# Optimization experiments

Measured on AMD Instinct MI355X. Metric: run time of the kernel, lower is better.

Reference implementation:

```python
import jax, jax.numpy as jnp
import numpy as np

B, T, C, H = 4, 4096, 1024, 64

def setup_inputs() -> dict:
    key = jax.random.key(0)
    kx, kq, kk, kv = jax.random.split(key, 4)
    x = jax.random.normal(kx, (B, T, C), dtype=jnp.float32)
    scale = 1.0 / np.sqrt(C)
    Wq = jax.random.normal(kq, (C, H), dtype=jnp.float32) * scale
    Wk = jax.random.normal(kk, (C, H), dtype=jnp.float32) * scale
    Wv = jax.random.normal(kv, (C, H), dtype=jnp.float32) * scale
    return {"x": x, "Wq": Wq, "Wk": Wk, "Wv": Wv}

def reference(x, Wq, Wk, Wv):
    Bsz, Tlen, _ = x.shape
    head_size = Wq.shape[1]
    q = x @ Wq  # [B,T,H]
    k = x @ Wk
    v = x @ Wv
    # scores [B,T,T], scaled by sqrt(head_size)
    scores = jnp.einsum('bqh,bkh->bqk', q, k) / jnp.sqrt(jnp.float32(head_size))
    causal = jnp.tril(jnp.ones((Tlen, Tlen), dtype=bool))
    scores = jnp.where(causal, scores, -jnp.inf)
    weights = jax.nn.softmax(scores, axis=-1)
    # dropout p=0.0 -> identity
    return jnp.einsum('bqk,bkh->bqh', weights, v)
```

## Files before the change

### kernel.cpp

```cpp
#include <hip/hip_runtime.h>
#include <hip/hip_bf16.h>

typedef __attribute__((ext_vector_type(8))) short short8;
typedef __attribute__((ext_vector_type(4))) float f32x4;

#define MFMA16(a, b, c) __builtin_amdgcn_mfma_f32_16x16x32_bf16((a), (b), (c), 0, 0, 0)

typedef const __attribute__((address_space(1))) unsigned int* gas_t;
typedef __attribute__((address_space(3))) unsigned int* las_t;
#define GLDS16(g, l) __builtin_amdgcn_global_load_lds((gas_t)(g), (las_t)(l), 16, 0, 0)

__device__ inline unsigned short f2bf(float f) {
    union { float f; unsigned int u; } v;
    v.f = f;
    unsigned int u = v.u;
    return (unsigned short)((u + 0x7fffu + ((u >> 16) & 1u)) >> 16);
}

__device__ inline float bf2f(unsigned short u) {
    union { unsigned int u; float f; } v;
    v.u = ((unsigned int)u) << 16;
    return v.f;
}

__device__ inline size_t WF(int n, int c) {
    return ((((size_t)(n >> 4)) * 32 + (c >> 5)) * 64 + ((c >> 3) & 3) * 16 + (n & 15)) * 8 + (c & 7);
}
__device__ inline size_t QKF(int q, int h) {
    return ((((size_t)(q >> 4)) * 2 + (h >> 5)) * 64 + ((h >> 3) & 3) * 16 + (q & 15)) * 8 + (h & 7);
}
__device__ inline size_t VF(int h, int t) {
    return ((((size_t)(h >> 4)) * 128 + (t >> 5)) * 64 + ((t >> 3) & 3) * 16 + (h & 15)) * 8 + (t & 7);
}

__global__ __launch_bounds__(256) void prep_w(const float* __restrict__ Wq,
                                              const float* __restrict__ Wk,
                                              const float* __restrict__ Wv,
                                              unsigned short* __restrict__ Wt) {
    int idx = blockIdx.x * 256 + threadIdx.x;
    if (idx >= 192 * 1024) return;
    int n = idx >> 10;
    int c = idx & 1023;
    const float* W = (n < 64) ? Wq : ((n < 128) ? Wk : Wv);
    float v = W[c * 64 + (n & 63)];
    if (n < 64) v *= 0.125f;
    Wt[WF(n, c)] = f2bf(v);
}

__global__ __launch_bounds__(256, 2) void projt(const float* __restrict__ x,
                                                const unsigned short* __restrict__ Wt,
                                                unsigned short* __restrict__ Qs,
                                                unsigned short* __restrict__ Ks,
                                                unsigned short* __restrict__ Vt) {
    __shared__ __align__(16) float xbuf[16 * 1024];

    const int tid = threadIdx.x;
    const int w = tid >> 6;
    const int lane = tid & 63;
    const int lr = lane & 15;
    const int lg = lane >> 4;
    const int t0 = blockIdx.x * 16;

#pragma unroll
    for (int rr = 0; rr < 4; rr++) {
        int r = w * 4 + rr;
#pragma unroll
        for (int q = 0; q < 4; q++) {
            int gc = q * 64 + (lane >> 4) * 16 + ((lane & 15) ^ r);
            const float* src = x + (size_t)(t0 + r) * 1024 + gc * 4;
            float* dst = &xbuf[r * 1024 + q * 256];
            GLDS16(src, dst);
        }
    }
    __syncthreads();

    f32x4 acc[3];
#pragma unroll
    for (int i = 0; i < 3; i++) acc[i] = (f32x4){0.f, 0.f, 0.f, 0.f};

    for (int t = 0; t < 8; ++t) {
        const int ch0 = t * 32;

        short8 bfr[4][3];
#pragma unroll
        for (int h = 0; h < 4; h++)
#pragma unroll
            for (int nt = 0; nt < 3; nt++)
                bfr[h][nt] = *(const short8*)(Wt +
                    (((size_t)(w * 3 + nt) * 32 + (t * 4 + h)) * 64 + lane) * 8);

#pragma unroll
        for (int h = 0; h < 4; h++) {
            int cb = ch0 + h * 8 + lg * 2;
            int l0 = (cb & ~15) | ((cb & 15) ^ lr);
            int l1 = ((cb + 1) & ~15) | (((cb + 1) & 15) ^ lr);
            float4 a0 = *(const float4*)&xbuf[lr * 1024 + l0 * 4];
            float4 a1 = *(const float4*)&xbuf[lr * 1024 + l1 * 4];
            short8 a;
            a[0] = (short)f2bf(a0.x); a[1] = (short)f2bf(a0.y);
            a[2] = (short)f2bf(a0.z); a[3] = (short)f2bf(a0.w);
            a[4] = (short)f2bf(a1.x); a[5] = (short)f2bf(a1.y);
            a[6] = (short)f2bf(a1.z); a[7] = (short)f2bf(a1.w);
#pragma unroll
            for (int nt = 0; nt < 3; nt++) acc[nt] = MFMA16(a, bfr[h][nt], acc[nt]);
        }
    }

    const int nbase = w * 48;
#pragma unroll
    for (int nt = 0; nt < 3; nt++) {
#pragma unroll
        for (int r = 0; r < 4; r++) {
            int n = nbase + nt * 16 + lr;
            int tq = t0 + lg * 4 + r;
            int b = tq >> 12;
            int qq = tq & 4095;
            unsigned short val = f2bf(acc[nt][r]);
            if (n < 64) {
                Qs[(size_t)b * 262144 + QKF(qq, n)] = val;
            } else if (n < 128) {
                Ks[(size_t)b * 262144 + QKF(qq, n - 64)] = val;
            } else {
                Vt[(size_t)b * 262144 + VF(n - 128, qq)] = val;
            }
        }
    }
}

#define SROW 72

template <int NS>
__global__ __launch_bounds__(64) void attn(const unsigned short* __restrict__ Qs,
                                           const unsigned short* __restrict__ Ks,
                                           const unsigned short* __restrict__ Vt,
                                           float* __restrict__ out,
                                           unsigned short* __restrict__ accP,
                                           float* __restrict__ mP,
                                           float* __restrict__ lP) {
    __shared__ unsigned short pl[32 * SROW];

    const int ntasks = 512 * NS;
    int raw = ntasks - 1 - blockIdx.x;
    int qt_g = raw / NS;
    int c = raw - qt_g * NS;
    int qt = qt_g >> 2;
    int b = qt_g & 3;
    int q0 = qt * 32;

    int lane = threadIdx.x;
    int lr = lane & 15;
    int lg = lane >> 4;

    const unsigned short* Qb = Qs + (size_t)b * 262144;
    const unsigned short* Kb = Ks + (size_t)b * 262144;
    const unsigned short* Vb = Vt + (size_t)b * 262144;

    short8 qf[2][2];
#pragma unroll
    for (int qs = 0; qs < 2; qs++)
#pragma unroll
        for (int kh = 0; kh < 2; kh++)
            qf[qs][kh] = *(const short8*)(Qb +
                (((size_t)((q0 >> 4) + qs) * 2 + kh) * 64 + lane) * 8);

    f32x4 acc[4][2];
#pragma unroll
    for (int i = 0; i < 4; i++)
#pragma unroll
        for (int qs = 0; qs < 2; qs++) acc[i][qs] = (f32x4){0.f, 0.f, 0.f, 0.f};
    float m[2] = {-1e30f, -1e30f};
    float l[2] = {0.f, 0.f};

    int nt = (q0 + 95) >> 6;
    int tb = (c * nt) / NS;
    int te = ((c + 1) * nt) / NS;

    short8 kf[4][2];
    if (tb < te) {
#pragma unroll
        for (int t = 0; t < 4; t++)
#pragma unroll
            for (int half = 0; half < 2; half++)
                kf[t][half] = *(const short8*)(Kb +
                    (((size_t)((tb * 64) >> 4) + t) * 2 + half) * 512 + lane * 8);
    }

    for (int t64 = tb; t64 < te; ++t64) {
        int kv0 = t64 * 64;

        f32x4 s[4][2];
#pragma unroll
        for (int t = 0; t < 4; t++)
#pragma unroll
            for (int qs = 0; qs < 2; qs++) {
                f32x4 z = (f32x4){0.f, 0.f, 0.f, 0.f};
                z = MFMA16(kf[t][0], qf[qs][0], z);
                z = MFMA16(kf[t][1], qf[qs][1], z);
                s[t][qs] = z;
            }

        short8 vf[4][2];
#pragma unroll
        for (int ht = 0; ht < 4; ht++)
#pragma unroll
            for (int half = 0; half < 2; half++)
                vf[ht][half] = *(const short8*)(Vb +
                    (((size_t)ht * 128 + (kv0 >> 5) + half) * 64 + lane) * 8);

        if (t64 + 1 < te) {
            int kvn = (t64 + 1) * 64;
#pragma unroll
            for (int t = 0; t < 4; t++)
#pragma unroll
                for (int half = 0; half < 2; half++)
                    kf[t][half] = *(const short8*)(Kb +
                        (((size_t)(kvn >> 4) + t) * 2 + half) * 512 + lane * 8);
        }

        if (kv0 + 63 > q0) {
#pragma unroll
            for (int t = 0; t < 4; t++)
#pragma unroll
                for (int qs = 0; qs < 2; qs++)
#pragma unroll
                    for (int r = 0; r < 4; r++) {
                        int kv = kv0 + t * 16 + lg * 4 + r;
                        if (kv > q0 + qs * 16 + lr) s[t][qs][r] = -1e30f;
                    }
        }

        float pmax[2] = {-1e30f, -1e30f};
#pragma unroll
        for (int t = 0; t < 4; t++)
#pragma unroll
            for (int qs = 0; qs < 2; qs++)
#pragma unroll
                for (int r = 0; r < 4; r++) pmax[qs] = fmaxf(pmax[qs], s[t][qs][r]);

        int ok = (pmax[0] <= m[0] + 8.0f) && (pmax[1] <= m[1] + 8.0f);
        if (!__all(ok)) {
            float alpha[2];
#pragma unroll
            for (int qs = 0; qs < 2; qs++) {
                float mx = pmax[qs];
                mx = fmaxf(mx, __shfl_xor(mx, 16));
                mx = fmaxf(mx, __shfl_xor(mx, 32));
                float mn = fmaxf(m[qs], mx);
                alpha[qs] = __expf(m[qs] - mn);
                m[qs] = mn;
                l[qs] *= alpha[qs];
            }
            float ar[2][4];
#pragma unroll
            for (int qs = 0; qs < 2; qs++)
#pragma unroll
                for (int r = 0; r < 4; r++) ar[qs][r] = __shfl(alpha[qs], lg * 4 + r);
#pragma unroll
            for (int ht = 0; ht < 4; ht++)
#pragma unroll
                for (int qs = 0; qs < 2; qs++)
#pragma unroll
                    for (int r = 0; r < 4; r++) acc[ht][qs][r] *= ar[qs][r];
        }

#pragma unroll
        for (int t = 0; t < 4; t++)
#pragma unroll
            for (int qs = 0; qs < 2; qs++)
#pragma unroll
                for (int r = 0; r < 4; r++) {
                    float e = __expf(s[t][qs][r] - m[qs]);
                    s[t][qs][r] = e;
                    l[qs] += e;
                }

#pragma unroll
        for (int qs = 0; qs < 2; qs++)
#pragma unroll
            for (int t = 0; t < 4; t++) {
                uint2 uu;
                uu.x = (unsigned)f2bf(s[t][qs][0]) | ((unsigned)f2bf(s[t][qs][1]) << 16);
                uu.y = (unsigned)f2bf(s[t][qs][2]) | ((unsigned)f2bf(s[t][qs][3]) << 16);
                *(uint2*)&pl[(qs * 16 + lr) * SROW + t * 16 + lg * 4] = uu;
            }
        asm volatile("s_waitcnt lgkmcnt(0)" ::: "memory");
        __builtin_amdgcn_sched_barrier(0);
        short8 pa[2][2];
#pragma unroll
        for (int qs = 0; qs < 2; qs++)
#pragma unroll
            for (int half = 0; half < 2; half++)
                pa[qs][half] = *(const short8*)&pl[(qs * 16 + lr) * SROW +
                                                   half * 32 + lg * 8];

#pragma unroll
        for (int ht = 0; ht < 4; ht++)
#pragma unroll
            for (int qs = 0; qs < 2; qs++) {
                acc[ht][qs] = MFMA16(pa[qs][0], vf[ht][0], acc[ht][qs]);
                acc[ht][qs] = MFMA16(pa[qs][1], vf[ht][1], acc[ht][qs]);
            }
    }

    float lt[2];
#pragma unroll
    for (int qs = 0; qs < 2; qs++) {
        float v = l[qs];
        v += __shfl_xor(v, 16);
        v += __shfl_xor(v, 32);
        lt[qs] = v;
    }

    if (NS == 1) {
        float rl[2][4];
#pragma unroll
        for (int qs = 0; qs < 2; qs++)
#pragma unroll
            for (int r = 0; r < 4; r++) rl[qs][r] = 1.0f / __shfl(lt[qs], lg * 4 + r);
#pragma unroll
        for (int ht = 0; ht < 4; ht++)
#pragma unroll
            for (int qs = 0; qs < 2; qs++)
#pragma unroll
                for (int r = 0; r < 4; r++) {
                    size_t o = ((size_t)b * 4096 + q0 + qs * 16 + lg * 4 + r) * 64 +
                               ht * 16 + lr;
                    out[o] = acc[ht][qs][r] * rl[qs][r];
                }
    } else {
        int tidx = qt_g * NS + c;
        unsigned short* ap = accP + (size_t)tidx * 2048;
#pragma unroll
        for (int ht = 0; ht < 4; ht++)
#pragma unroll
            for (int qs = 0; qs < 2; qs++)
#pragma unroll
                for (int r = 0; r < 4; r++)
                    ap[(qs * 16 + lg * 4 + r) * 64 + ht * 16 + lr] =
                        f2bf(acc[ht][qs][r]);
        if (lane < 16) {
#pragma unroll
            for (int qs = 0; qs < 2; qs++) {
                mP[tidx * 32 + qs * 16 + lane] = m[qs];
                lP[tidx * 32 + qs * 16 + lane] = lt[qs];
            }
        }
    }
}

template <int NS>
__global__ __launch_bounds__(256) void combine(const unsigned short* __restrict__ accP,
                                               const float* __restrict__ mP,
                                               const float* __restrict__ lP,
                                               float* __restrict__ out) {
    int g = blockIdx.x * 256 + threadIdx.x;
    int h = g & 63;
    int row = g >> 6;
    int b = row >> 12;
    int t = row & 4095;
    int qt = t >> 5;
    int qr = t & 31;
    int qt_g = qt * 4 + b;

    float mc[NS];
    float M = -1e30f;
#pragma unroll
    for (int c = 0; c < NS; c++) {
        mc[c] = mP[(qt_g * NS + c) * 32 + qr];
        M = fmaxf(M, mc[c]);
    }
    float num = 0.f, den = 0.f;
#pragma unroll
    for (int c = 0; c < NS; c++) {
        float wgt = __expf(mc[c] - M);
        den += wgt * lP[(qt_g * NS + c) * 32 + qr];
        num += wgt * bf2f(accP[(size_t)(qt_g * NS + c) * 2048 + qr * 64 + h]);
    }
    out[g] = num / den;
}

extern "C" void kernel_launch(void* const* d_in, const int* in_sizes, int n_in,
                              void* d_out, int out_size, void* d_ws, size_t ws_size,
                              hipStream_t stream) {
    const float* x  = (const float*)d_in[0];
    const float* Wq = (const float*)d_in[1];
    const float* Wk = (const float*)d_in[2];
    const float* Wv = (const float*)d_in[3];
    float* out = (float*)d_out;

    char* ws = (char*)d_ws;
    unsigned short* Qs = (unsigned short*)(ws);
    unsigned short* Ks = (unsigned short*)(ws + (2u << 20));
    unsigned short* Vt = (unsigned short*)(ws + (4u << 20));
    unsigned short* Wt = (unsigned short*)(ws + (6u << 20));
    unsigned short* accP = (unsigned short*)(ws + (8u << 20));
    float* mP = (float*)(ws + (24u << 20));
    float* lP = (float*)(ws + (24u << 20) + (512u << 10));

    prep_w<<<768, 256, 0, stream>>>(Wq, Wk, Wv, Wt);
    projt<<<1024, 256, 0, stream>>>(x, Wt, Qs, Ks, Vt);

    if (ws_size >= (25u << 20)) {
        attn<4><<<2048, 64, 0, stream>>>(Qs, Ks, Vt, out, accP, mP, lP);
        combine<4><<<4096, 256, 0, stream>>>(accP, mP, lP, out);
    } else {
        attn<1><<<512, 64, 0, stream>>>(Qs, Ks, Vt, out, accP, mP, lP);
    }
}
```

Before: 69.76 us.

## Stream x slabs through double-buffered LDS in the QKV projection kernel

```diff
diff --git a/kernel.cpp b/kernel.cpp
--- a/kernel.cpp
+++ b/kernel.cpp
@@ -5,10 +5,6 @@
 typedef __attribute__((ext_vector_type(4))) float f32x4;
 
 #define MFMA16(a, b, c) __builtin_amdgcn_mfma_f32_16x16x32_bf16((a), (b), (c), 0, 0, 0)
-
-typedef const __attribute__((address_space(1))) unsigned int* gas_t;
-typedef __attribute__((address_space(3))) unsigned int* las_t;
-#define GLDS16(g, l) __builtin_amdgcn_global_load_lds((gas_t)(g), (las_t)(l), 16, 0, 0)
 
 __device__ inline unsigned short f2bf(float f) {
     union { float f; unsigned int u; } v;
@@ -47,12 +43,12 @@
     Wt[WF(n, c)] = f2bf(v);
 }
 
-__global__ __launch_bounds__(256, 2) void projt(const float* __restrict__ x,
+__global__ __launch_bounds__(256, 4) void projt(const float* __restrict__ x,
                                                 const unsigned short* __restrict__ Wt,
                                                 unsigned short* __restrict__ Qs,
                                                 unsigned short* __restrict__ Ks,
                                                 unsigned short* __restrict__ Vt) {
-    __shared__ __align__(16) float xbuf[16 * 1024];
+    __shared__ __align__(16) float xbuf[2][16 * 128];
 
     const int tid = threadIdx.x;
     const int w = tid >> 6;
@@ -61,49 +57,69 @@
     const int lg = lane >> 4;
     const int t0 = blockIdx.x * 16;
 
-#pragma unroll
-    for (int rr = 0; rr < 4; rr++) {
-        int r = w * 4 + rr;
-#pragma unroll
-        for (int q = 0; q < 4; q++) {
-            int gc = q * 64 + (lane >> 4) * 16 + ((lane & 15) ^ r);
-            const float* src = x + (size_t)(t0 + r) * 1024 + gc * 4;
-            float* dst = &xbuf[r * 1024 + q * 256];
-            GLDS16(src, dst);
-        }
-    }
-    __syncthreads();
+    const int srow0 = w * 4 + (lane >> 5);
+    const int schunk = lane & 31;
+
+#define LOADSLAB(v, sl)                                                         \
+    {                                                                           \
+        const uint4* xr = (const uint4*)(x + (size_t)(t0) * 1024 + (sl) * 128); \
+        v[0] = xr[(size_t)(srow0) * 256 + schunk];                              \
+        v[1] = xr[(size_t)(srow0 + 2) * 256 + schunk];                          \
+    }
+
+#define DSWRITE(buf, v)                                                         \
+    {                                                                           \
+        _Pragma("unroll")                                                       \
+        for (int j = 0; j < 2; j++) {                                           \
+            int row = srow0 + j * 2;                                            \
+            int l = (schunk & ~15) | ((schunk & 15) ^ (row & 15));              \
+            *(uint4*)&xbuf[buf][row * 128 + l * 4] = v[j];                      \
+        }                                                                       \
+    }
+
+    uint4 vc[2], vn[2];
+    LOADSLAB(vc, 0);
+    DSWRITE(0, vc);
+    LOADSLAB(vc, 1);
 
     f32x4 acc[3];
 #pragma unroll
     for (int i = 0; i < 3; i++) acc[i] = (f32x4){0.f, 0.f, 0.f, 0.f};
 
+#pragma unroll
     for (int t = 0; t < 8; ++t) {
-        const int ch0 = t * 32;
-
-        short8 bfr[4][3];
-#pragma unroll
-        for (int h = 0; h < 4; h++)
+        if (t + 2 < 8) LOADSLAB(vn, t + 2);
+
+        asm volatile("s_waitcnt lgkmcnt(0)" ::: "memory");
+        __builtin_amdgcn_sched_barrier(0);
+        __builtin_amdgcn_s_barrier();
+        __builtin_amdgcn_sched_barrier(0);
+
+        if (t + 1 < 8) DSWRITE((t + 1) & 1, vc);
+
+        const float* xb = &xbuf[t & 1][0];
+#pragma unroll
+        for (int h = 0; h < 4; h++) {
+            short8 bfr[3];
 #pragma unroll
             for (int nt = 0; nt < 3; nt++)
-                bfr[h][nt] = *(const short8*)(Wt +
+                bfr[nt] = *(const short8*)(Wt +
                     (((size_t)(w * 3 + nt) * 32 + (t * 4 + h)) * 64 + lane) * 8);
-
-#pragma unroll
-        for (int h = 0; h < 4; h++) {
-            int cb = ch0 + h * 8 + lg * 2;
+            int cb = h * 8 + lg * 2;
             int l0 = (cb & ~15) | ((cb & 15) ^ lr);
             int l1 = ((cb + 1) & ~15) | (((cb + 1) & 15) ^ lr);
-            float4 a0 = *(const float4*)&xbuf[lr * 1024 + l0 * 4];
-            float4 a1 = *(const float4*)&xbuf[lr * 1024 + l1 * 4];
+            float4 a0 = *(const float4*)&xb[lr * 128 + l0 * 4];
+            float4 a1 = *(const float4*)&xb[lr * 128 + l1 * 4];
             short8 a;
             a[0] = (short)f2bf(a0.x); a[1] = (short)f2bf(a0.y);
             a[2] = (short)f2bf(a0.z); a[3] = (short)f2bf(a0.w);
             a[4] = (short)f2bf(a1.x); a[5] = (short)f2bf(a1.y);
             a[6] = (short)f2bf(a1.z); a[7] = (short)f2bf(a1.w);
 #pragma unroll
-            for (int nt = 0; nt < 3; nt++) acc[nt] = MFMA16(a, bfr[h][nt], acc[nt]);
-        }
+            for (int nt = 0; nt < 3; nt++) acc[nt] = MFMA16(a, bfr[nt], acc[nt]);
+        }
+
+        if (t + 2 < 8) { vc[0] = vn[0]; vc[1] = vn[1]; }
     }
 
     const int nbase = w * 48;
```

Result: faster. 64.19 us (-8.0%).
